# Kernel tuning notes

Hardware: AMD Instinct MI355X
Metric: run time of the kernel (lower is better)

The kernel has to match this reference:

```python
import jax, jax.numpy as jnp
import numpy as np
from jax import lax

FEAT_STRIDE = 16
PRE_NMS_TOPN = 2000
POST_NMS_TOPN = 300
NMS_THRESH = 0.7
MIN_SIZE = 16.0
IMG_H, IMG_W = 1600.0, 2400.0


def _generate_anchors(base_size=16, ratios=(0.5, 1.0, 2.0), scales=(8, 16, 32)):
    w = h = float(base_size)
    xc = yc = 0.5 * (base_size - 1)
    size = w * h
    out = []
    for r in ratios:
        ws = np.round(np.sqrt(size / r))
        hs = np.round(ws * r)
        for s in scales:
            W, H = ws * s, hs * s
            out.append([xc - 0.5 * (W - 1), yc - 0.5 * (H - 1),
                        xc + 0.5 * (W - 1), yc + 0.5 * (H - 1)])
    return np.array(out, dtype=np.float32)  # [9,4]

ANCHORS = jnp.asarray(_generate_anchors())


def _conv(x, w, b, padding):
    y = lax.conv_general_dilated(x, w, (1, 1), padding,
                                 dimension_numbers=('NCHW', 'OIHW', 'NCHW'))
    return y + b[None, :, None, None]


def _nms_mask(boxes, thresh):
    # greedy NMS over score-sorted boxes; returns keep mask
    N = boxes.shape[0]
    x1, y1, x2, y2 = boxes[:, 0], boxes[:, 1], boxes[:, 2], boxes[:, 3]
    areas = (x2 - x1 + 1.0) * (y2 - y1 + 1.0)
    idx = jnp.arange(N)

    def body(i, supp):
        xx1 = jnp.maximum(x1[i], x1)
        yy1 = jnp.maximum(y1[i], y1)
        xx2 = jnp.minimum(x2[i], x2)
        yy2 = jnp.minimum(y2[i], y2)
        w = jnp.maximum(xx2 - xx1 + 1.0, 0.0)
        h = jnp.maximum(yy2 - yy1 + 1.0, 0.0)
        inter = w * h
        iou = inter / (areas[i] + areas - inter)
        cond = (iou > thresh) & (idx > i) & jnp.logical_not(supp[i])
        return supp | cond

    supp = lax.fori_loop(0, N, body, jnp.zeros((N,), dtype=bool))
    return jnp.logical_not(supp)


def reference(features, conv1_w, conv1_b, score_w, score_b, bbox_w, bbox_b, img_info):
    # RPN head
    x = jax.nn.relu(_conv(features, conv1_w, conv1_b, 'SAME'))
    cls = _conv(x, score_w, score_b, 'VALID')    # [1, 2A, H, W]
    deltas = _conv(x, bbox_w, bbox_b, 'VALID')   # [1, 4A, H, W]
    N, C, H, W = cls.shape
    A = C // 2
    # reshape_layer to [N,2,A*H,W], softmax over dim 1, reshape back
    prob = jax.nn.softmax(cls.reshape(N, 2, A * H, W), axis=1).reshape(N, C, H, W)
    fg = prob[:, A:, :, :]                                  # foreground probs
    scores = fg.transpose(0, 2, 3, 1).reshape(-1)           # (H*W*A,)
    d = deltas.transpose(0, 2, 3, 1).reshape(-1, 4)         # (H*W*A, 4)

    # anchor grid (h-major, w-minor, anchor-minor) matching the transpose order
    shift_x = jnp.arange(W, dtype=jnp.float32) * FEAT_STRIDE
    shift_y = jnp.arange(H, dtype=jnp.float32) * FEAT_STRIDE
    sx, sy = jnp.meshgrid(shift_x, shift_y)                 # [H,W]
    shifts = jnp.stack([sx.ravel(), sy.ravel(), sx.ravel(), sy.ravel()], axis=1)
    anchors = (ANCHORS[None, :, :] + shifts[:, None, :]).reshape(-1, 4)

    # bbox_transform_inv decode
    ws = anchors[:, 2] - anchors[:, 0] + 1.0
    hs = anchors[:, 3] - anchors[:, 1] + 1.0
    cx = anchors[:, 0] + 0.5 * ws
    cy = anchors[:, 1] + 0.5 * hs
    pcx = d[:, 0] * ws + cx
    pcy = d[:, 1] * hs + cy
    pw = jnp.exp(d[:, 2]) * ws
    ph = jnp.exp(d[:, 3]) * hs
    props = jnp.stack([pcx - 0.5 * pw, pcy - 0.5 * ph,
                       pcx + 0.5 * pw, pcy + 0.5 * ph], axis=1)
    # clip to image
    props = jnp.stack([jnp.clip(props[:, 0], 0.0, img_info[1] - 1.0),
                       jnp.clip(props[:, 1], 0.0, img_info[0] - 1.0),
                       jnp.clip(props[:, 2], 0.0, img_info[1] - 1.0),
                       jnp.clip(props[:, 3], 0.0, img_info[0] - 1.0)], axis=1)

    # min-size filter (masked, jit-friendly)
    bw = props[:, 2] - props[:, 0] + 1.0
    bh = props[:, 3] - props[:, 1] + 1.0
    min_sz = MIN_SIZE * img_info[2]
    valid = (bw >= min_sz) & (bh >= min_sz)
    scores = jnp.where(valid, scores, -jnp.inf)

    # pre-NMS top-k (sorted desc)
    top_scores, order = lax.top_k(scores, PRE_NMS_TOPN)
    boxes = props[order]
    keep = _nms_mask(boxes, NMS_THRESH)
    kept_scores = jnp.where(keep, top_scores, -jnp.inf)
    post_scores, kidx = lax.top_k(kept_scores, POST_NMS_TOPN)
    final = boxes[kidx]
    rois = jnp.concatenate([jnp.zeros((POST_NMS_TOPN, 1), final.dtype), final], axis=1)
    return rois, post_scores


def setup_inputs() -> dict:
    key = jax.random.key(0)
    ks = jax.random.split(key, 4)
    H, W = 100, 150  # 1600x2400 image at stride 16
    features = jax.random.normal(ks[0], (1, 512, H, W), dtype=jnp.float32)
    conv1_w = jax.random.normal(ks[1], (512, 512, 3, 3), dtype=jnp.float32) * 0.01
    conv1_b = jnp.zeros((512,), dtype=jnp.float32)
    score_w = jax.random.normal(ks[2], (18, 512, 1, 1), dtype=jnp.float32) * 0.01
    score_b = jnp.zeros((18,), dtype=jnp.float32)
    bbox_w = jax.random.normal(ks[3], (36, 512, 1, 1), dtype=jnp.float32) * 0.001
    bbox_b = jnp.zeros((36,), dtype=jnp.float32)
    img_info = jnp.array([IMG_H, IMG_W, 1.0], dtype=jnp.float32)
    return {"features": features, "conv1_w": conv1_w, "conv1_b": conv1_b,
            "score_w": score_w, "score_b": score_b,
            "bbox_w": bbox_w, "bbox_b": bbox_b, "img_info": img_info}
```

## Files before the change

### kernel.cpp

```cpp
#include <hip/hip_runtime.h>
#include <math.h>

#define Hh 100
#define Ww 150
#define Mm 15000
#define NP 135000

typedef double f64x4 __attribute__((ext_vector_type(4)));

#if defined(__HIP_DEVICE_COMPILE__)
#if __has_builtin(__builtin_amdgcn_mfma_f64_16x16x4f64)
#define MFMA64(a,b,c) __builtin_amdgcn_mfma_f64_16x16x4f64((a),(b),(c),0,0,0)
#elif __has_builtin(__builtin_amdgcn_mfma_f64_16x16x4_f64)
#define MFMA64(a,b,c) __builtin_amdgcn_mfma_f64_16x16x4_f64((a),(b),(c),0,0,0)
#else
#error "no f64 mfma builtin on device"
#endif
#define GLOAD4(g,l) __builtin_amdgcn_global_load_lds( \
    (const __attribute__((address_space(1))) unsigned*)(g), \
    (__attribute__((address_space(3))) unsigned*)(l), 4, 0, 0)
#else
#define MFMA64(a,b,c) (c)
#define GLOAD4(g,l) ((void)(g),(void)(l))
#endif

__constant__ double ANCH[9][4] = {
  {-84.0,-40.0,99.0,55.0},{-176.0,-88.0,191.0,103.0},{-360.0,-184.0,375.0,191.0},
  {-56.0,-56.0,71.0,71.0},{-120.0,-120.0,135.0,135.0},{-248.0,-248.0,263.0,263.0},
  {-36.0,-80.0,51.0,95.0},{-80.0,-168.0,95.0,183.0},{-168.0,-344.0,183.0,359.0}};

__global__ __launch_bounds__(256) void prep_wT(const float* __restrict__ w,
                                               float* __restrict__ wT) {
  __shared__ float t[32][32][10];
  const int co0 = blockIdx.x * 32, ci0 = blockIdx.y * 32;
  for (int e = threadIdx.x; e < 9216; e += 256) {
    int cr = e / 288;
    int rem = e - cr * 288;
    int cir = rem / 9, tap = rem - cir * 9;
    t[cir][cr][tap] = w[(size_t)(co0 + cr) * 4608 + (ci0 + cir) * 9 + tap];
  }
  __syncthreads();
  for (int e = threadIdx.x; e < 9216; e += 256) {
    int tap = e / 1024;
    int rem = e - tap * 1024;
    int cir = rem >> 5, cr = rem & 31;
    wT[(size_t)tap * 262144 + (size_t)(ci0 + cir) * 512 + (co0 + cr)] = t[cir][cr][tap];
  }
}

__global__ void prep_w54(const float* __restrict__ sw, const float* __restrict__ bw,
                         double* __restrict__ w54) {
  int idx = blockIdx.x * 256 + threadIdx.x;
  if (idx < 54 * 512) {
    int o = idx >> 9, c = idx & 511;
    w54[idx] = (double)((o < 18) ? sw[o * 512 + c] : bw[(o - 18) * 512 + c]);
  }
}

__global__ __launch_bounds__(256, 4) void conv3x3(const float* __restrict__ feat,
                                                  const float* __restrict__ wT,
                                                  const float* __restrict__ bias,
                                                  const float* __restrict__ zp,
                                                  float* __restrict__ x) {
  __shared__ union {
    struct { float A[2][32][72]; float B[2][32][136]; } s;
    float Lx[128][65];
  } sm;
  const int tid = threadIdx.x;
  const int lane = tid & 63;
  const int wv = tid >> 6;
  const int pw = (wv & 1) * 32;
  const int cw = (wv >> 1) * 64;
  const int m0 = blockIdx.x * 64;
  const int n0 = blockIdx.y * 128;
  const int l15 = lane & 15, l4 = lane >> 4;

  f64x4 zero; zero[0] = 0.0; zero[1] = 0.0; zero[2] = 0.0; zero[3] = 0.0;
  f64x4 acc[2][4];
#pragma unroll
  for (int i = 0; i < 2; ++i)
#pragma unroll
    for (int q = 0; q < 4; ++q) acc[i][q] = zero;

  const int ka = wv * 8;
  const int ma = m0 + lane;
  const int ha = ma / 150, wa = ma - ha * 150;

  auto stage = [&](int cn, int buf) {
    const int tap = cn >> 4;
    const int cb = (cn & 15) << 5;
    const int t3 = tap / 3;
    const int dy = t3 - 1, dx = tap - t3 * 3 - 1;
    const int hh = ha + dy, wwp = wa + dx;
    const bool ok = (ma < Mm) && (hh >= 0) && (hh < Hh) && (wwp >= 0) && (wwp < Ww);
    const int src = ok ? (hh * Ww + wwp) : 0;
    const float* ab = feat + (size_t)(cb + ka) * Mm + src;
#pragma unroll
    for (int kk = 0; kk < 8; ++kk)
      GLOAD4(ok ? (ab + (size_t)kk * Mm) : zp, &sm.s.A[buf][ka + kk][0]);
    const float* wbase = wT + (size_t)tap * 262144 + (size_t)(cb + ka) * 512 + n0 + lane;
#pragma unroll
    for (int kk = 0; kk < 8; ++kk) {
      GLOAD4(wbase + (size_t)kk * 512,      &sm.s.B[buf][ka + kk][0]);
      GLOAD4(wbase + (size_t)kk * 512 + 64, &sm.s.B[buf][ka + kk][64]);
    }
  };

  stage(0, 0);
  __syncthreads();

  for (int c = 0; c < 144; ++c) {
    const int b = c & 1;
    if (c + 1 < 144) stage(c + 1, b ^ 1);
#pragma unroll
    for (int t = 0; t < 8; ++t) {
      const int kt = t * 4 + l4;
      const double a0 = (double)sm.s.A[b][kt][pw + l15];
      const double a1 = (double)sm.s.A[b][kt][pw + 16 + l15];
      const double b0 = (double)sm.s.B[b][kt][cw + l15];
      const double b1 = (double)sm.s.B[b][kt][cw + 16 + l15];
      const double b2 = (double)sm.s.B[b][kt][cw + 32 + l15];
      const double b3 = (double)sm.s.B[b][kt][cw + 48 + l15];
      acc[0][0] = MFMA64(a0, b0, acc[0][0]);
      acc[0][1] = MFMA64(a0, b1, acc[0][1]);
      acc[0][2] = MFMA64(a0, b2, acc[0][2]);
      acc[0][3] = MFMA64(a0, b3, acc[0][3]);
      acc[1][0] = MFMA64(a1, b0, acc[1][0]);
      acc[1][1] = MFMA64(a1, b1, acc[1][1]);
      acc[1][2] = MFMA64(a1, b2, acc[1][2]);
      acc[1][3] = MFMA64(a1, b3, acc[1][3]);
    }
    __syncthreads();
  }

  const double ap1 = (l4 == 0) ? (double)l15 : 0.0;
  const double bp1 = (l4 == 0) ? 1.0 : 0.0;
  const f64x4 rowp = MFMA64(ap1, bp1, zero);
  const double ap2 = (l4 == 0) ? 1.0 : 0.0;
  const double bp2 = (l4 == 0) ? (double)l15 : 0.0;
  const f64x4 colp = MFMA64(ap2, bp2, zero);

#pragma unroll
  for (int i = 0; i < 2; ++i)
#pragma unroll
    for (int q = 0; q < 4; ++q)
#pragma unroll
      for (int r = 0; r < 4; ++r) {
        const int row = pw + i * 16 + (int)rowp[r];
        const int col = cw + q * 16 + (int)colp[r];
        const double v = acc[i][q][r] + (double)bias[n0 + col];
        sm.Lx[col][row] = (float)(v > 0.0 ? v : 0.0);
      }
  __syncthreads();
  for (int e = tid; e < 64 * 128; e += 256) {
    const int co = e >> 6, p = e & 63;
    const int m = m0 + p;
    if (m < Mm) x[(size_t)(n0 + co) * Mm + m] = sm.Lx[co][p];
  }
}

__global__ __launch_bounds__(256) void conv1x1(const float* __restrict__ x,
                                               const double* __restrict__ w54,
                                               const float* __restrict__ sb,
                                               const float* __restrict__ bb,
                                               float* __restrict__ cls,
                                               float* __restrict__ dl) {
  int m = blockIdx.x * 256 + threadIdx.x;
  int g = blockIdx.y;
  double acc[9];
#pragma unroll
  for (int o = 0; o < 9; ++o) acc[o] = 0.0;
  if (m < Mm) {
    const double* wg = w54 + (size_t)g * 9 * 512;
    for (int c = 0; c < 512; ++c) {
      double v = (double)x[(size_t)c * Mm + m];
#pragma unroll
      for (int o = 0; o < 9; ++o) acc[o] += v * wg[o * 512 + c];
    }
#pragma unroll
    for (int o = 0; o < 9; ++o) {
      int oo = g * 9 + o;
      if (oo < 18) cls[oo * Mm + m] = (float)(acc[o] + (double)sb[oo]);
      else dl[(oo - 18) * Mm + m] = (float)(acc[o] + (double)bb[oo - 18]);
    }
  }
}

__global__ void decode(const float* __restrict__ cls, const float* __restrict__ dl,
                       const float* __restrict__ info, double4* __restrict__ props,
                       float* __restrict__ scoresF, unsigned long long* __restrict__ keys64,
                       unsigned* __restrict__ keys32, unsigned* __restrict__ hist) {
  int i = blockIdx.x * 256 + threadIdx.x;
  if (i >= NP) return;
  int m = i / 9, a = i - m * 9;
  int h = m / 150, w = m - h * 150;
  double c0 = (double)cls[a * Mm + m], c1 = (double)cls[(9 + a) * Mm + m];
  double mx = fmax(c0, c1);
  double e0 = exp(c0 - mx), e1 = exp(c1 - mx);
  double p = e1 / (e0 + e1);
  double d0 = (double)dl[(a * 4 + 0) * Mm + m], d1 = (double)dl[(a * 4 + 1) * Mm + m];
  double d2 = (double)dl[(a * 4 + 2) * Mm + m], d3 = (double)dl[(a * 4 + 3) * Mm + m];
  double sx = (double)w * 16.0, sy = (double)h * 16.0;
  double ax1 = ANCH[a][0] + sx, ay1 = ANCH[a][1] + sy;
  double ax2 = ANCH[a][2] + sx, ay2 = ANCH[a][3] + sy;
  double aw = ax2 - ax1 + 1.0, ah = ay2 - ay1 + 1.0;
  double cx = ax1 + 0.5 * aw, cy = ay1 + 0.5 * ah;
  double pcx = d0 * aw + cx, pcy = d1 * ah + cy;
  double pw = exp(d2) * aw, ph = exp(d3) * ah;
  double x1 = pcx - 0.5 * pw, y1 = pcy - 0.5 * ph;
  double x2 = pcx + 0.5 * pw, y2 = pcy + 0.5 * ph;
  double IH = (double)info[0], IW = (double)info[1], sc = (double)info[2];
  x1 = fmin(fmax(x1, 0.0), IW - 1.0); y1 = fmin(fmax(y1, 0.0), IH - 1.0);
  x2 = fmin(fmax(x2, 0.0), IW - 1.0); y2 = fmin(fmax(y2, 0.0), IH - 1.0);
  double bwd = x2 - x1 + 1.0, bhd = y2 - y1 + 1.0;
  bool valid = (bwd >= 16.0 * sc) && (bhd >= 16.0 * sc);
  double score = valid ? p : -__builtin_inf();
  double4 pr; pr.x = x1; pr.y = y1; pr.z = x2; pr.w = y2;
  props[i] = pr;
  float pf = (float)score;
  scoresF[i] = pf;
  unsigned long long b = (unsigned long long)__double_as_longlong(score);
  unsigned long long s = (b >> 63) ? ~b : (b | 0x8000000000000000ull);
  unsigned long long k = ~s;
  keys64[i] = (k & ~0x3FFFFull) | (unsigned long long)i;
  unsigned ub = __float_as_uint(pf);
  unsigned us = (ub >> 31) ? ~ub : (ub | 0x80000000u);
  unsigned k32 = ~us;
  keys32[i] = k32;
  atomicAdd(&hist[k32 >> 16], 1u);
}

__global__ __launch_bounds__(1024) void cutoff_k(const unsigned* __restrict__ hist,
                                                 int* __restrict__ Bout) {
  __shared__ unsigned ps[1024];
  int t = threadIdx.x;
  unsigned s = 0;
  for (int b = t * 64; b < t * 64 + 64; ++b) s += hist[b];
  ps[t] = s; __syncthreads();
  for (int off = 1; off < 1024; off <<= 1) {
    unsigned a = ps[t];
    unsigned bb2 = (t >= off) ? ps[t - off] : 0u;
    __syncthreads();
    ps[t] = a + bb2;
    __syncthreads();
  }
  unsigned excl = ps[t] - s;
  if (excl < 2000u) {
    unsigned run = excl;
    for (int b = t * 64; b < t * 64 + 64; ++b) {
      unsigned nb = run + hist[b];
      if (run < 2000u && nb >= 2000u) *Bout = b;
      run = nb;
    }
  }
}

__global__ void compact_k(const unsigned* __restrict__ keys32,
                          const unsigned long long* __restrict__ keys64,
                          const int* __restrict__ Bptr,
                          unsigned long long* __restrict__ cand, int* __restrict__ cnt) {
  int i = blockIdx.x * 256 + threadIdx.x;
  if (i >= NP) return;
  int B = *Bptr;
  if ((int)(keys32[i] >> 16) <= B) {
    int pos = atomicAdd(cnt, 1);
    if (pos < 8192) cand[pos] = keys64[i];
  }
}

__global__ __launch_bounds__(1024) void sort_top(const unsigned long long* __restrict__ cand,
                                                 const int* __restrict__ pcnt,
                                                 const double4* __restrict__ props,
                                                 const float* __restrict__ scoresF,
                                                 double4* __restrict__ boxes2000,
                                                 float* __restrict__ score2000) {
  __shared__ unsigned long long sh[8192];
  int t = threadIdx.x;
  int cnt = *pcnt; if (cnt > 8192) cnt = 8192;
  for (int i = t; i < 8192; i += 1024) sh[i] = (i < cnt) ? cand[i] : ~0ull;
  __syncthreads();
  for (int kb = 1; kb <= 13; ++kb) {
    int k = 1 << kb;
    for (int jb = kb - 1; jb >= 0; --jb) {
      int j = 1 << jb;
      for (int s = t; s < 4096; s += 1024) {
        int i = ((s >> jb) << (jb + 1)) | (s & (j - 1));
        int l = i + j;
        bool up = ((i & k) == 0);
        unsigned long long a = sh[i], b = sh[l];
        if (up ? (a > b) : (a < b)) { sh[i] = b; sh[l] = a; }
      }
      __syncthreads();
    }
  }
  for (int r = t; r < 2000; r += 1024) {
    unsigned long long key = sh[r];
    int idx = (int)(key & 0x3FFFFull);
    boxes2000[r] = props[idx];
    score2000[r] = scoresF[idx];
  }
}

__global__ __launch_bounds__(256) void nms_mask(const double4* __restrict__ boxes,
                                                unsigned long long* __restrict__ mask) {
  int tid = threadIdx.x;
  int r = blockIdx.x * 8 + (tid >> 5);
  int wd = tid & 31;
  double4 bi = boxes[r];
  double ai = (bi.z - bi.x + 1.0) * (bi.w - bi.y + 1.0);
  unsigned long long bits = 0;
  int j0 = wd * 64;
  int jmax = 2000 - j0; if (jmax > 64) jmax = 64;
  for (int jj = 0; jj < jmax; ++jj) {
    int j = j0 + jj;
    if (j > r) {
      double4 bj = boxes[j];
      double xx1 = fmax(bi.x, bj.x), yy1 = fmax(bi.y, bj.y);
      double xx2 = fmin(bi.z, bj.z), yy2 = fmin(bi.w, bj.w);
      double w_ = fmax(xx2 - xx1 + 1.0, 0.0), h_ = fmax(yy2 - yy1 + 1.0, 0.0);
      double inter = w_ * h_;
      double aj = (bj.z - bj.x + 1.0) * (bj.w - bj.y + 1.0);
      double iou = inter / (ai + aj - inter);
      if (iou > 0.7) bits |= 1ull << jj;
    }
  }
  mask[r * 32 + wd] = bits;
}

__global__ __launch_bounds__(256) void suppress(const unsigned long long* __restrict__ mask,
                                                unsigned long long* __restrict__ aliveOut) {
  __shared__ unsigned long long rows[64][32];
  int tid = threadIdx.x;
  int lane = tid & 63;
  unsigned long long myword = 0;
  if (tid < 64) {
    if (lane < 31) myword = ~0ull;
    else if (lane == 31) myword = 0xFFFFull;
  }
  for (int c = 0; c < 32; ++c) {
    __syncthreads();
    for (int idx = tid; idx < 2048; idx += 256) {
      int g = c * 2048 + idx;
      ((unsigned long long*)rows)[idx] = (g < 64000) ? mask[g] : 0ull;
    }
    __syncthreads();
    if (tid < 64) {
      for (int r = 0; r < 64; ++r) {
        int i = c * 64 + r;
        unsigned long long rw = rows[r][lane & 31];
        unsigned long long aw = __shfl(myword, i >> 6);
        if ((aw >> (i & 63)) & 1ull) {
          if (lane < 32) myword &= ~rw;
        }
      }
    }
  }
  __syncthreads();
  if (tid < 32) aliveOut[tid] = myword;
}

__global__ __launch_bounds__(1024) void finalize(const unsigned long long* __restrict__ alive,
                                                 const double4* __restrict__ boxes,
                                                 const float* __restrict__ scores,
                                                 float* __restrict__ out) {
  __shared__ int ps[1024];
  int t = threadIdx.x;
  int e0 = 2 * t, e1 = 2 * t + 1;
  int f0 = (e0 < 2000) ? (int)((alive[e0 >> 6] >> (e0 & 63)) & 1ull) : 0;
  int f1 = (e1 < 2000) ? (int)((alive[e1 >> 6] >> (e1 & 63)) & 1ull) : 0;
  int v = f0 + f1;
  ps[t] = v; __syncthreads();
  for (int off = 1; off < 1024; off <<= 1) {
    int a = ps[t];
    int b = (t >= off) ? ps[t - off] : 0;
    __syncthreads();
    ps[t] = a + b;
    __syncthreads();
  }
  int incl = ps[t];
  int excl = incl - v;
  int Na = ps[1023];
  if (f0 && excl < 300) {
    double4 bx = boxes[e0];
    out[excl * 5 + 0] = 0.f; out[excl * 5 + 1] = (float)bx.x; out[excl * 5 + 2] = (float)bx.y;
    out[excl * 5 + 3] = (float)bx.z; out[excl * 5 + 4] = (float)bx.w;
    out[1500 + excl] = scores[e0];
  }
  int p1 = excl + f0;
  if (f1 && p1 < 300) {
    double4 bx = boxes[e1];
    out[p1 * 5 + 0] = 0.f; out[p1 * 5 + 1] = (float)bx.x; out[p1 * 5 + 2] = (float)bx.y;
    out[p1 * 5 + 3] = (float)bx.z; out[p1 * 5 + 4] = (float)bx.w;
    out[1500 + p1] = scores[e1];
  }
  if (Na < 300) {
    if (e0 < 2000 && !f0) {
      int q = Na + (e0 - excl);
      if (q < 300) {
        double4 bx = boxes[e0];
        out[q * 5 + 0] = 0.f; out[q * 5 + 1] = (float)bx.x; out[q * 5 + 2] = (float)bx.y;
        out[q * 5 + 3] = (float)bx.z; out[q * 5 + 4] = (float)bx.w;
        out[1500 + q] = -__builtin_inff();
      }
    }
    if (e1 < 2000 && !f1) {
      int q = Na + (e1 - (excl + f0));
      if (q < 300) {
        double4 bx = boxes[e1];
        out[q * 5 + 0] = 0.f; out[q * 5 + 1] = (float)bx.x; out[q * 5 + 2] = (float)bx.y;
        out[q * 5 + 3] = (float)bx.z; out[q * 5 + 4] = (float)bx.w;
        out[1500 + q] = -__builtin_inff();
      }
    }
  }
}

extern "C" void kernel_launch(void* const* d_in, const int* in_sizes, int n_in,
                              void* d_out, int out_size, void* d_ws, size_t ws_size,
                              hipStream_t stream) {
  (void)in_sizes; (void)n_in; (void)out_size; (void)ws_size;
  const float* feat = (const float*)d_in[0];
  const float* w1   = (const float*)d_in[1];
  const float* b1   = (const float*)d_in[2];
  const float* sw   = (const float*)d_in[3];
  const float* sb   = (const float*)d_in[4];
  const float* bw   = (const float*)d_in[5];
  const float* bb   = (const float*)d_in[6];
  const float* info = (const float*)d_in[7];
  float* out = (float*)d_out;

  char* ws = (char*)d_ws;
  size_t off = 0;
  auto alloc = [&](size_t bytes) -> void* {
    void* p = ws + off;
    off += (bytes + 255) & ~(size_t)255;
    return p;
  };
  float* x        = (float*)alloc((size_t)512 * Mm * 4);
  float* wT       = (float*)alloc((size_t)9 * 512 * 512 * 4);
  double* w54     = (double*)alloc((size_t)54 * 512 * 8);
  float* cls      = (float*)alloc((size_t)18 * Mm * 4);
  float* dl       = (float*)alloc((size_t)36 * Mm * 4);
  double4* props  = (double4*)alloc((size_t)NP * 32);
  float* scoresF  = (float*)alloc((size_t)NP * 4);
  unsigned long long* keys64 = (unsigned long long*)alloc((size_t)NP * 8);
  unsigned* keys32 = (unsigned*)alloc((size_t)NP * 4);
  unsigned* hist   = (unsigned*)alloc((size_t)65536 * 4);
  int* Bptr        = (int*)alloc(256);
  int* cnt         = (int*)alloc(256);
  unsigned long long* cand = (unsigned long long*)alloc((size_t)8192 * 8);
  double4* boxes2000 = (double4*)alloc((size_t)2000 * 32);
  float* score2000   = (float*)alloc((size_t)2000 * 4);
  unsigned long long* mask  = (unsigned long long*)alloc((size_t)2000 * 32 * 8);
  unsigned long long* alive = (unsigned long long*)alloc((size_t)32 * 8);
  float* zp        = (float*)alloc(256);

  hipMemsetAsync(hist, 0, 65536 * 4, stream);
  hipMemsetAsync(cnt, 0, 4, stream);
  hipMemsetAsync(zp, 0, 256, stream);

  prep_wT<<<dim3(16, 16), 256, 0, stream>>>(w1, wT);
  prep_w54<<<108, 256, 0, stream>>>(sw, bw, w54);
  conv3x3<<<dim3(235, 4), 256, 0, stream>>>(feat, wT, b1, zp, x);
  conv1x1<<<dim3(59, 6), 256, 0, stream>>>(x, w54, sb, bb, cls, dl);
  decode<<<528, 256, 0, stream>>>(cls, dl, info, props, scoresF, keys64, keys32, hist);
  cutoff_k<<<1, 1024, 0, stream>>>(hist, Bptr);
  compact_k<<<528, 256, 0, stream>>>(keys32, keys64, Bptr, cand, cnt);
  sort_top<<<1, 1024, 0, stream>>>(cand, cnt, props, scoresF, boxes2000, score2000);
  nms_mask<<<250, 256, 0, stream>>>(boxes2000, mask);
  suppress<<<1, 256, 0, stream>>>(mask, alive);
  finalize<<<1, 1024, 0, stream>>>(alive, boxes2000, score2000, out);
}
```

Before: 2.033 ms.

## Repartition conv3x3 wave tiles to 16 pixels by 128 channels and zero-fill padding in LDS

Each of the four waves now covers 16 pixels across all 128 output channels, replacing the previous 32 pixel by 64 channel split. Per k-step a wave does one A LDS read and eight B reads instead of two A and four B reads, keeping eight MFMAs per step. Out-of-bounds halo pixels are now written as zeros to LDS directly rather than loaded from a zero page through global_load_lds, which removes the zp buffer and its memset. The change in LDS read volume and the wave-divergent zero-fill branch are the main trade-offs.

```diff
diff --git a/kernel.cpp b/kernel.cpp
--- a/kernel.cpp
+++ b/kernel.cpp
@@ -60,7 +60,6 @@
 __global__ __launch_bounds__(256, 4) void conv3x3(const float* __restrict__ feat,
                                                   const float* __restrict__ wT,
                                                   const float* __restrict__ bias,
-                                                  const float* __restrict__ zp,
                                                   float* __restrict__ x) {
   __shared__ union {
     struct { float A[2][32][72]; float B[2][32][136]; } s;
@@ -69,18 +68,15 @@
   const int tid = threadIdx.x;
   const int lane = tid & 63;
   const int wv = tid >> 6;
-  const int pw = (wv & 1) * 32;
-  const int cw = (wv >> 1) * 64;
+  const int pxw = wv * 16;
   const int m0 = blockIdx.x * 64;
   const int n0 = blockIdx.y * 128;
   const int l15 = lane & 15, l4 = lane >> 4;
 
   f64x4 zero; zero[0] = 0.0; zero[1] = 0.0; zero[2] = 0.0; zero[3] = 0.0;
-  f64x4 acc[2][4];
-#pragma unroll
-  for (int i = 0; i < 2; ++i)
-#pragma unroll
-    for (int q = 0; q < 4; ++q) acc[i][q] = zero;
+  f64x4 acc[8];
+#pragma unroll
+  for (int q = 0; q < 8; ++q) acc[q] = zero;
 
   const int ka = wv * 8;
   const int ma = m0 + lane;
@@ -93,11 +89,15 @@
     const int dy = t3 - 1, dx = tap - t3 * 3 - 1;
     const int hh = ha + dy, wwp = wa + dx;
     const bool ok = (ma < Mm) && (hh >= 0) && (hh < Hh) && (wwp >= 0) && (wwp < Ww);
-    const int src = ok ? (hh * Ww + wwp) : 0;
-    const float* ab = feat + (size_t)(cb + ka) * Mm + src;
-#pragma unroll
-    for (int kk = 0; kk < 8; ++kk)
-      GLOAD4(ok ? (ab + (size_t)kk * Mm) : zp, &sm.s.A[buf][ka + kk][0]);
+    if (!ok) {
+#pragma unroll
+      for (int kk = 0; kk < 8; ++kk) sm.s.A[buf][ka + kk][lane] = 0.0f;
+    } else {
+      const float* ab = feat + (size_t)(cb + ka) * Mm + (hh * Ww + wwp);
+#pragma unroll
+      for (int kk = 0; kk < 8; ++kk)
+        GLOAD4(ab + (size_t)kk * Mm, &sm.s.A[buf][ka + kk][0]);
+    }
     const float* wbase = wT + (size_t)tap * 262144 + (size_t)(cb + ka) * 512 + n0 + lane;
 #pragma unroll
     for (int kk = 0; kk < 8; ++kk) {
@@ -115,20 +115,12 @@
 #pragma unroll
     for (int t = 0; t < 8; ++t) {
       const int kt = t * 4 + l4;
-      const double a0 = (double)sm.s.A[b][kt][pw + l15];
-      const double a1 = (double)sm.s.A[b][kt][pw + 16 + l15];
-      const double b0 = (double)sm.s.B[b][kt][cw + l15];
-      const double b1 = (double)sm.s.B[b][kt][cw + 16 + l15];
-      const double b2 = (double)sm.s.B[b][kt][cw + 32 + l15];
-      const double b3 = (double)sm.s.B[b][kt][cw + 48 + l15];
-      acc[0][0] = MFMA64(a0, b0, acc[0][0]);
-      acc[0][1] = MFMA64(a0, b1, acc[0][1]);
-      acc[0][2] = MFMA64(a0, b2, acc[0][2]);
-      acc[0][3] = MFMA64(a0, b3, acc[0][3]);
-      acc[1][0] = MFMA64(a1, b0, acc[1][0]);
-      acc[1][1] = MFMA64(a1, b1, acc[1][1]);
-      acc[1][2] = MFMA64(a1, b2, acc[1][2]);
-      acc[1][3] = MFMA64(a1, b3, acc[1][3]);
+      const double a = (double)sm.s.A[b][kt][pxw + l15];
+#pragma unroll
+      for (int q = 0; q < 8; ++q) {
+        const double bq = (double)sm.s.B[b][kt][q * 16 + l15];
+        acc[q] = MFMA64(a, bq, acc[q]);
+      }
     }
     __syncthreads();
   }
@@ -141,16 +133,14 @@
   const f64x4 colp = MFMA64(ap2, bp2, zero);
 
 #pragma unroll
-  for (int i = 0; i < 2; ++i)
-#pragma unroll
-    for (int q = 0; q < 4; ++q)
-#pragma unroll
-      for (int r = 0; r < 4; ++r) {
-        const int row = pw + i * 16 + (int)rowp[r];
-        const int col = cw + q * 16 + (int)colp[r];
-        const double v = acc[i][q][r] + (double)bias[n0 + col];
-        sm.Lx[col][row] = (float)(v > 0.0 ? v : 0.0);
-      }
+  for (int q = 0; q < 8; ++q)
+#pragma unroll
+    for (int r = 0; r < 4; ++r) {
+      const int row = pxw + (int)rowp[r];
+      const int col = q * 16 + (int)colp[r];
+      const double v = acc[q][r] + (double)bias[n0 + col];
+      sm.Lx[col][row] = (float)(v > 0.0 ? v : 0.0);
+    }
   __syncthreads();
   for (int e = tid; e < 64 * 128; e += 256) {
     const int co = e >> 6, p = e & 63;
@@ -453,15 +443,13 @@
   float* score2000   = (float*)alloc((size_t)2000 * 4);
   unsigned long long* mask  = (unsigned long long*)alloc((size_t)2000 * 32 * 8);
   unsigned long long* alive = (unsigned long long*)alloc((size_t)32 * 8);
-  float* zp        = (float*)alloc(256);
 
   hipMemsetAsync(hist, 0, 65536 * 4, stream);
   hipMemsetAsync(cnt, 0, 4, stream);
-  hipMemsetAsync(zp, 0, 256, stream);
 
   prep_wT<<<dim3(16, 16), 256, 0, stream>>>(w1, wT);
   prep_w54<<<108, 256, 0, stream>>>(sw, bw, w54);
-  conv3x3<<<dim3(235, 4), 256, 0, stream>>>(feat, wT, b1, zp, x);
+  conv3x3<<<dim3(235, 4), 256, 0, stream>>>(feat, wT, b1, x);
   conv1x1<<<dim3(59, 6), 256, 0, stream>>>(x, w54, sb, bb, cls, dl);
   decode<<<528, 256, 0, stream>>>(cls, dl, info, props, scoresF, keys64, keys32, hist);
   cutoff_k<<<1, 1024, 0, stream>>>(hist, Bptr);
```

After: 2.001 ms. About the same (-1.6%).

## Warp-specialize conv3x3 into producer and MFMA consumer wavefronts

Applied to the files above, without the earlier changes.

The 3x3 conv kernel grows to 512 threads. Four wavefronts now only run f64 MFMA work, and four producer wavefronts stage the next A/B tile into LDS using ordinary register loads, with float4 loads for weights, in place of global_load_lds. The goal is to take load issue off the compute waves so it overlaps with the math. In exchange, block size and register pressure rise, which can cut occupancy, and A-tile loads become scalar global loads followed by LDS stores.

```diff
diff --git a/kernel.cpp b/kernel.cpp
--- a/kernel.cpp
+++ b/kernel.cpp
@@ -16,12 +16,8 @@
 #else
 #error "no f64 mfma builtin on device"
 #endif
-#define GLOAD4(g,l) __builtin_amdgcn_global_load_lds( \
-    (const __attribute__((address_space(1))) unsigned*)(g), \
-    (__attribute__((address_space(3))) unsigned*)(l), 4, 0, 0)
 #else
 #define MFMA64(a,b,c) (c)
-#define GLOAD4(g,l) ((void)(g),(void)(l))
 #endif
 
 __constant__ double ANCH[9][4] = {
@@ -57,10 +53,9 @@
   }
 }
 
-__global__ __launch_bounds__(256, 4) void conv3x3(const float* __restrict__ feat,
+__global__ __launch_bounds__(512, 4) void conv3x3(const float* __restrict__ feat,
                                                   const float* __restrict__ wT,
                                                   const float* __restrict__ bias,
-                                                  const float* __restrict__ zp,
                                                   float* __restrict__ x) {
   __shared__ union {
     struct { float A[2][32][72]; float B[2][32][136]; } s;
@@ -69,90 +64,102 @@
   const int tid = threadIdx.x;
   const int lane = tid & 63;
   const int wv = tid >> 6;
-  const int pw = (wv & 1) * 32;
-  const int cw = (wv >> 1) * 64;
   const int m0 = blockIdx.x * 64;
   const int n0 = blockIdx.y * 128;
   const int l15 = lane & 15, l4 = lane >> 4;
 
   f64x4 zero; zero[0] = 0.0; zero[1] = 0.0; zero[2] = 0.0; zero[3] = 0.0;
-  f64x4 acc[2][4];
-#pragma unroll
-  for (int i = 0; i < 2; ++i)
-#pragma unroll
-    for (int q = 0; q < 4; ++q) acc[i][q] = zero;
-
-  const int ka = wv * 8;
-  const int ma = m0 + lane;
-  const int ha = ma / 150, wa = ma - ha * 150;
-
-  auto stage = [&](int cn, int buf) {
-    const int tap = cn >> 4;
-    const int cb = (cn & 15) << 5;
-    const int t3 = tap / 3;
-    const int dy = t3 - 1, dx = tap - t3 * 3 - 1;
-    const int hh = ha + dy, wwp = wa + dx;
-    const bool ok = (ma < Mm) && (hh >= 0) && (hh < Hh) && (wwp >= 0) && (wwp < Ww);
-    const int src = ok ? (hh * Ww + wwp) : 0;
-    const float* ab = feat + (size_t)(cb + ka) * Mm + src;
-#pragma unroll
-    for (int kk = 0; kk < 8; ++kk)
-      GLOAD4(ok ? (ab + (size_t)kk * Mm) : zp, &sm.s.A[buf][ka + kk][0]);
-    const float* wbase = wT + (size_t)tap * 262144 + (size_t)(cb + ka) * 512 + n0 + lane;
-#pragma unroll
-    for (int kk = 0; kk < 8; ++kk) {
-      GLOAD4(wbase + (size_t)kk * 512,      &sm.s.B[buf][ka + kk][0]);
-      GLOAD4(wbase + (size_t)kk * 512 + 64, &sm.s.B[buf][ka + kk][64]);
-    }
-  };
-
-  stage(0, 0);
+
+  if (wv < 4) {
+    const int pw = (wv & 1) * 32;
+    const int cw = (wv >> 1) * 64;
+    f64x4 acc[2][4];
+#pragma unroll
+    for (int i = 0; i < 2; ++i)
+#pragma unroll
+      for (int q = 0; q < 4; ++q) acc[i][q] = zero;
+
+    __syncthreads();
+
+    for (int c = 0; c < 144; ++c) {
+      const int b = c & 1;
+#pragma unroll
+      for (int t = 0; t < 8; ++t) {
+        const int kt = t * 4 + l4;
+        const double a0 = (double)sm.s.A[b][kt][pw + l15];
+        const double a1 = (double)sm.s.A[b][kt][pw + 16 + l15];
+        const double b0 = (double)sm.s.B[b][kt][cw + l15];
+        const double b1 = (double)sm.s.B[b][kt][cw + 16 + l15];
+        const double b2 = (double)sm.s.B[b][kt][cw + 32 + l15];
+        const double b3 = (double)sm.s.B[b][kt][cw + 48 + l15];
+        acc[0][0] = MFMA64(a0, b0, acc[0][0]);
+        acc[0][1] = MFMA64(a0, b1, acc[0][1]);
+        acc[0][2] = MFMA64(a0, b2, acc[0][2]);
+        acc[0][3] = MFMA64(a0, b3, acc[0][3]);
+        acc[1][0] = MFMA64(a1, b0, acc[1][0]);
+        acc[1][1] = MFMA64(a1, b1, acc[1][1]);
+        acc[1][2] = MFMA64(a1, b2, acc[1][2]);
+        acc[1][3] = MFMA64(a1, b3, acc[1][3]);
+      }
+      __syncthreads();
+    }
+
+    const double ap1 = (l4 == 0) ? (double)l15 : 0.0;
+    const double bp1 = (l4 == 0) ? 1.0 : 0.0;
+    const f64x4 rowp = MFMA64(ap1, bp1, zero);
+    const double ap2 = (l4 == 0) ? 1.0 : 0.0;
+    const double bp2 = (l4 == 0) ? (double)l15 : 0.0;
+    const f64x4 colp = MFMA64(ap2, bp2, zero);
+
+#pragma unroll
+    for (int i = 0; i < 2; ++i)
+#pragma unroll
+      for (int q = 0; q < 4; ++q)
+#pragma unroll
+        for (int r = 0; r < 4; ++r) {
+          const int row = pw + i * 16 + (int)rowp[r];
+          const int col = cw + q * 16 + (int)colp[r];
+          const double v = acc[i][q][r] + (double)bias[n0 + col];
+          sm.Lx[col][row] = (float)(v > 0.0 ? v : 0.0);
+        }
+  } else {
+    const int ptid = tid - 256;
+    const int pa = ptid & 63;
+    const int ka = (ptid >> 6) * 8;
+    const int ma = m0 + pa;
+    const int ha = ma / 150, wa = ma - ha * 150;
+    const int cq = ptid & 31;
+    const int kb = (ptid >> 5) * 4;
+
+    auto stage = [&](int cn, int buf) {
+      const int tap = cn >> 4;
+      const int cb = (cn & 15) << 5;
+      const int t3 = tap / 3;
+      const int dy = t3 - 1, dx = tap - t3 * 3 - 1;
+      const int hh = ha + dy, wwp = wa + dx;
+      const bool ok = (ma < Mm) && (hh >= 0) && (hh < Hh) && (wwp >= 0) && (wwp < Ww);
+      const int src = hh * Ww + wwp;
+#pragma unroll
+      for (int kk = 0; kk < 8; ++kk)
+        sm.s.A[buf][ka + kk][pa] = ok ? feat[(size_t)(cb + ka + kk) * Mm + src] : 0.0f;
+      const float* wb = wT + (size_t)tap * 262144 + n0;
+#pragma unroll
+      for (int kk = 0; kk < 4; ++kk)
+        *(float4*)&sm.s.B[buf][kb + kk][cq * 4] =
+            *(const float4*)&wb[(size_t)(cb + kb + kk) * 512 + cq * 4];
+    };
+
+    stage(0, 0);
+    __syncthreads();
+
+    for (int c = 0; c < 144; ++c) {
+      if (c + 1 < 144) stage(c + 1, (c + 1) & 1);
+      __syncthreads();
+    }
+  }
+
   __syncthreads();
-
-  for (int c = 0; c < 144; ++c) {
-    const int b = c & 1;
-    if (c + 1 < 144) stage(c + 1, b ^ 1);
-#pragma unroll
-    for (int t = 0; t < 8; ++t) {
-      const int kt = t * 4 + l4;
-      const double a0 = (double)sm.s.A[b][kt][pw + l15];
-      const double a1 = (double)sm.s.A[b][kt][pw + 16 + l15];
-      const double b0 = (double)sm.s.B[b][kt][cw + l15];
-      const double b1 = (double)sm.s.B[b][kt][cw + 16 + l15];
-      const double b2 = (double)sm.s.B[b][kt][cw + 32 + l15];
-      const double b3 = (double)sm.s.B[b][kt][cw + 48 + l15];
-      acc[0][0] = MFMA64(a0, b0, acc[0][0]);
-      acc[0][1] = MFMA64(a0, b1, acc[0][1]);
-      acc[0][2] = MFMA64(a0, b2, acc[0][2]);
-      acc[0][3] = MFMA64(a0, b3, acc[0][3]);
-      acc[1][0] = MFMA64(a1, b0, acc[1][0]);
-      acc[1][1] = MFMA64(a1, b1, acc[1][1]);
-      acc[1][2] = MFMA64(a1, b2, acc[1][2]);
-      acc[1][3] = MFMA64(a1, b3, acc[1][3]);
-    }
-    __syncthreads();
-  }
-
-  const double ap1 = (l4 == 0) ? (double)l15 : 0.0;
-  const double bp1 = (l4 == 0) ? 1.0 : 0.0;
-  const f64x4 rowp = MFMA64(ap1, bp1, zero);
-  const double ap2 = (l4 == 0) ? 1.0 : 0.0;
-  const double bp2 = (l4 == 0) ? (double)l15 : 0.0;
-  const f64x4 colp = MFMA64(ap2, bp2, zero);
-
-#pragma unroll
-  for (int i = 0; i < 2; ++i)
-#pragma unroll
-    for (int q = 0; q < 4; ++q)
-#pragma unroll
-      for (int r = 0; r < 4; ++r) {
-        const int row = pw + i * 16 + (int)rowp[r];
-        const int col = cw + q * 16 + (int)colp[r];
-        const double v = acc[i][q][r] + (double)bias[n0 + col];
-        sm.Lx[col][row] = (float)(v > 0.0 ? v : 0.0);
-      }
-  __syncthreads();
-  for (int e = tid; e < 64 * 128; e += 256) {
+  for (int e = tid; e < 64 * 128; e += 512) {
     const int co = e >> 6, p = e & 63;
     const int m = m0 + p;
     if (m < Mm) x[(size_t)(n0 + co) * Mm + m] = sm.Lx[co][p];
@@ -453,15 +460,13 @@
   float* score2000   = (float*)alloc((size_t)2000 * 4);
   unsigned long long* mask  = (unsigned long long*)alloc((size_t)2000 * 32 * 8);
   unsigned long long* alive = (unsigned long long*)alloc((size_t)32 * 8);
-  float* zp        = (float*)alloc(256);
 
   hipMemsetAsync(hist, 0, 65536 * 4, stream);
   hipMemsetAsync(cnt, 0, 4, stream);
-  hipMemsetAsync(zp, 0, 256, stream);
 
   prep_wT<<<dim3(16, 16), 256, 0, stream>>>(w1, wT);
   prep_w54<<<108, 256, 0, stream>>>(sw, bw, w54);
-  conv3x3<<<dim3(235, 4), 256, 0, stream>>>(feat, wT, b1, zp, x);
+  conv3x3<<<dim3(235, 4), 512, 0, stream>>>(feat, wT, b1, x);
   conv1x1<<<dim3(59, 6), 256, 0, stream>>>(x, w54, sb, bb, cls, dl);
   decode<<<528, 256, 0, stream>>>(cls, dl, info, props, scoresF, keys64, keys32, hist);
   cutoff_k<<<1, 1024, 0, stream>>>(hist, Bptr);
```

Result: faster. 1.852 ms (-8.9%).
